# Optimization experiments

Measured on AMD Instinct MI355X. Metric: run time of the kernel, lower is better.

Reference implementation:

```python
import jax, jax.numpy as jnp
import numpy as np
from jax.scipy.special import logsumexp

TAU = 0.05
N_ITERS = 10
LR = 0.5
BETA1 = 0.9
BETA2 = 0.999
EPS_ADAM = 1e-8
BATCH, N, M = 16, 1024, 1024


def setup_inputs() -> dict:
    key = jax.random.key(0)
    k1, k2, k3 = jax.random.split(key, 3)
    log_alpha = jax.random.normal(k1, (BATCH, N, M), dtype=jnp.float32)
    # valid log-marginals (rows of log_alpha's transport plan must sum to exp(log_a))
    log_a = jax.nn.log_softmax(jax.random.normal(k2, (BATCH, N), dtype=jnp.float32), axis=-1)
    log_b = jax.nn.log_softmax(jax.random.normal(k3, (BATCH, M), dtype=jnp.float32), axis=-1)
    return {"log_alpha": log_alpha, "log_a": log_a, "log_b": log_b}


def _sinkhorn_adam(log_alpha, log_a, log_b):
    kernel = log_alpha / TAU  # [B, N, M]
    b, n, m = log_alpha.shape
    u = jnp.zeros((b, n), dtype=log_alpha.dtype)
    v = jnp.zeros((b, m), dtype=log_alpha.dtype)
    m_u = jnp.zeros_like(u)
    v_u = jnp.zeros_like(u)
    m_v = jnp.zeros_like(v)
    v_v = jnp.zeros_like(v)

    def step(carry, iter_idx):
        u, v, m_u, v_u, m_v, v_v = carry
        t = (iter_idx + 1).astype(log_alpha.dtype)
        bc1 = 1.0 - jnp.power(jnp.asarray(BETA1, log_alpha.dtype), t)
        bc2 = 1.0 - jnp.power(jnp.asarray(BETA2, log_alpha.dtype), t)

        # u update (Adam on the fixed-point residual)
        u_target = log_a - logsumexp(kernel + v[:, None, :], axis=-1)
        g_u = u_target - u
        m_u = BETA1 * m_u + (1.0 - BETA1) * g_u
        v_u = BETA2 * v_u + (1.0 - BETA2) * (g_u * g_u)
        u_next = u + LR * (m_u / bc1) / (jnp.sqrt(v_u / bc2) + EPS_ADAM)

        # v update using the fresh u
        v_target = log_b - logsumexp(kernel + u_next[:, :, None], axis=-2)
        g_v = v_target - v
        m_v = BETA1 * m_v + (1.0 - BETA1) * g_v
        v_v = BETA2 * v_v + (1.0 - BETA2) * (g_v * g_v)
        v_next = v + LR * (m_v / bc1) / (jnp.sqrt(v_v / bc2) + EPS_ADAM)

        return (u_next, v_next, m_u, v_u, m_v, v_v), None

    (u, v, m_u, v_u, m_v, v_v), _ = jax.lax.scan(
        step, (u, v, m_u, v_u, m_v, v_v), jnp.arange(N_ITERS))
    # transport plan
    return jnp.exp(kernel + u[:, :, None] + v[:, None, :])


def reference(log_alpha, log_a, log_b):
    return _sinkhorn_adam(log_alpha, log_a, log_b)
```

## Files before the change

kernel.cpp:

```cpp
#include <hip/hip_runtime.h>
#include <cmath>

#define BB 16
#define NN 1024
#define MM 1024
#define RPB 8
#define NSLAB (NN / RPB)

static constexpr float INV_TAU = 20.0f;
static constexpr float LR   = 0.5f;
static constexpr float B1f  = 0.9f;
static constexpr float B2f  = 0.999f;
static constexpr float EPSA = 1e-8f;
static constexpr float EXP_CAP = 88.0f;

#define OFF_U   0
#define OFF_V   16384
#define OFF_MU  32768
#define OFF_VU  49152
#define OFF_MV  65536
#define OFF_VV  81920
#define OFF_PART 98304

__global__ void init_state(float* __restrict__ ws) {
    int i = blockIdx.x * 256 + threadIdx.x;
    ws[i] = 0.0f;
}

__global__ __launch_bounds__(256, 4) void iter_fused(
    const float* __restrict__ la, const float* __restrict__ log_a,
    float* __restrict__ ws, float2* __restrict__ part,
    float bc1, float bc2)
{
    const int slab = blockIdx.x;
    const int b    = blockIdx.y;
    const int row0 = slab * RPB;
    const int tid  = threadIdx.x;
    const int wave = tid >> 6;
    const int lane = tid & 63;
    __shared__ float redm[4 * RPB];
    __shared__ float reds[4 * RPB];
    __shared__ float fin[RPB];
    __shared__ float su[RPB];

    const float* Kb = la + ((size_t)b * NN + row0) * MM + 4 * tid;
    float kr[RPB][4];
#pragma unroll
    for (int r = 0; r < RPB; ++r) {
        const float4 k4 = *(const float4*)(Kb + (size_t)r * MM);
        kr[r][0] = k4.x * INV_TAU; kr[r][1] = k4.y * INV_TAU;
        kr[r][2] = k4.z * INV_TAU; kr[r][3] = k4.w * INV_TAU;
    }
    const float4 v4 = *(const float4*)(ws + OFF_V + b * MM + 4 * tid);
    const float vj[4] = {v4.x, v4.y, v4.z, v4.w};

    float pm[RPB];
#pragma unroll
    for (int r = 0; r < RPB; ++r)
        pm[r] = fmaxf(fmaxf(kr[r][0] + vj[0], kr[r][1] + vj[1]),
                      fmaxf(kr[r][2] + vj[2], kr[r][3] + vj[3]));
#pragma unroll
    for (int off = 32; off; off >>= 1)
#pragma unroll
        for (int r = 0; r < RPB; ++r)
            pm[r] = fmaxf(pm[r], __shfl_xor(pm[r], off, 64));
    if (lane == 0)
#pragma unroll
        for (int r = 0; r < RPB; ++r) redm[wave * RPB + r] = pm[r];
    __syncthreads();
    if (tid < RPB)
        fin[tid] = fmaxf(fmaxf(redm[tid], redm[RPB + tid]),
                         fmaxf(redm[2 * RPB + tid], redm[3 * RPB + tid]));
    __syncthreads();
    float Mr[RPB];
#pragma unroll
    for (int r = 0; r < RPB; ++r) Mr[r] = fin[r];

    float ps[RPB];
#pragma unroll
    for (int r = 0; r < RPB; ++r)
        ps[r] = __expf(kr[r][0] + vj[0] - Mr[r]) + __expf(kr[r][1] + vj[1] - Mr[r])
              + __expf(kr[r][2] + vj[2] - Mr[r]) + __expf(kr[r][3] + vj[3] - Mr[r]);
#pragma unroll
    for (int off = 32; off; off >>= 1)
#pragma unroll
        for (int r = 0; r < RPB; ++r)
            ps[r] += __shfl_xor(ps[r], off, 64);
    if (lane == 0)
#pragma unroll
        for (int r = 0; r < RPB; ++r) reds[wave * RPB + r] = ps[r];
    __syncthreads();
    if (tid < RPB) {
        const int r  = tid;
        const int gi = b * NN + row0 + r;
        const float S   = reds[r] + reds[RPB + r] + reds[2 * RPB + r] + reds[3 * RPB + r];
        const float lse = Mr[r] + __logf(S);
        const float uo  = ws[OFF_U + gi];
        const float gu  = (log_a[gi] - lse) - uo;
        const float m_  = B1f * ws[OFF_MU + gi] + (1.f - B1f) * gu;
        const float v_  = B2f * ws[OFF_VU + gi] + (1.f - B2f) * gu * gu;
        ws[OFF_MU + gi] = m_;
        ws[OFF_VU + gi] = v_;
        const float un  = uo + LR * (m_ / bc1) / (sqrtf(v_ / bc2) + EPSA);
        ws[OFF_U + gi]  = un;
        su[r] = un;
    }
    __syncthreads();
    float uu[RPB];
#pragma unroll
    for (int r = 0; r < RPB; ++r) uu[r] = su[r];

    float2 out4[4];
#pragma unroll
    for (int j = 0; j < 4; ++j) {
        float m = kr[0][j] + uu[0];
#pragma unroll
        for (int r = 1; r < RPB; ++r) m = fmaxf(m, kr[r][j] + uu[r]);
        float s = 0.f;
#pragma unroll
        for (int r = 0; r < RPB; ++r) s += __expf(kr[r][j] + uu[r] - m);
        out4[j] = make_float2(m, s);
    }
    float2* p = part + ((size_t)b * NSLAB + slab) * MM + 4 * tid;
    p[0] = out4[0]; p[1] = out4[1]; p[2] = out4[2]; p[3] = out4[3];
}

__global__ __launch_bounds__(256, 8) void combine(
    const float* __restrict__ log_b, float* __restrict__ ws,
    const float2* __restrict__ part, float bc1, float bc2)
{
    const int b   = blockIdx.x >> 4;
    const int mg  = blockIdx.x & 15;
    const int tid = threadIdx.x;
    const int c   = tid & 63;
    const int q   = tid >> 6;
    const int m   = mg * 64 + c;
    __shared__ float2 red[4][64];

    const float2* p = part + ((size_t)b * NSLAB + q * 32) * MM + m;
    float M = -3.0e38f, S = 0.f;
#pragma unroll 8
    for (int s = 0; s < 32; ++s) {
        const float2 pr = p[(size_t)s * MM];
        const float mn = fmaxf(M, pr.x);
        S = S * __expf(M - mn) + pr.y * __expf(pr.x - mn);
        M = mn;
    }
    red[q][c] = make_float2(M, S);
    __syncthreads();
    if (q == 0) {
        const float2 a = red[0][c], bb = red[1][c], cc = red[2][c], d = red[3][c];
        const float Mt = fmaxf(fmaxf(a.x, bb.x), fmaxf(cc.x, d.x));
        const float St = a.y * __expf(a.x - Mt) + bb.y * __expf(bb.x - Mt)
                       + cc.y * __expf(cc.x - Mt) + d.y * __expf(d.x - Mt);
        const int i = b * MM + m;
        const float lse = Mt + __logf(St);
        const float vo  = ws[OFF_V + i];
        const float gv  = (log_b[i] - lse) - vo;
        const float m_  = B1f * ws[OFF_MV + i] + (1.f - B1f) * gv;
        const float v_  = B2f * ws[OFF_VV + i] + (1.f - B2f) * gv * gv;
        ws[OFF_MV + i] = m_;
        ws[OFF_VV + i] = v_;
        ws[OFF_V + i]  = vo + LR * (m_ / bc1) / (sqrtf(v_ / bc2) + EPSA);
    }
}

__global__ void finalize(const float* __restrict__ la, const float* __restrict__ ws,
                         float* __restrict__ out)
{
    const size_t i4 = (size_t)blockIdx.x * 256 + threadIdx.x;
    const size_t e  = i4 * 4;
    const int row = (int)(e >> 10);
    const int b   = row >> 10;
    const int m   = (int)(e & 1023);
    const float uu = ws[OFF_U + row];
    const float4 k4 = ((const float4*)la)[i4];
    const float4 v4 = *(const float4*)(ws + OFF_V + b * MM + m);
    float4 o;
    o.x = __expf(fminf(k4.x * INV_TAU + uu + v4.x, EXP_CAP));
    o.y = __expf(fminf(k4.y * INV_TAU + uu + v4.y, EXP_CAP));
    o.z = __expf(fminf(k4.z * INV_TAU + uu + v4.z, EXP_CAP));
    o.w = __expf(fminf(k4.w * INV_TAU + uu + v4.w, EXP_CAP));
    ((float4*)out)[i4] = o;
}

extern "C" void kernel_launch(void* const* d_in, const int* in_sizes, int n_in,
                              void* d_out, int out_size, void* d_ws, size_t ws_size,
                              hipStream_t stream) {
    const float* la    = (const float*)d_in[0];
    const float* log_a = (const float*)d_in[1];
    const float* log_b = (const float*)d_in[2];
    float*  out  = (float*)d_out;
    float*  ws   = (float*)d_ws;
    float2* part = (float2*)(ws + OFF_PART);

    init_state<<<384, 256, 0, stream>>>(ws);
    for (int t = 1; t <= 10; ++t) {
        const float bc1 = 1.0f - powf(B1f, (float)t);
        const float bc2 = 1.0f - powf(B2f, (float)t);
        iter_fused<<<dim3(NSLAB, BB), 256, 0, stream>>>(la, log_a, ws, part, bc1, bc2);
        combine<<<BB * MM / 256, 256, 0, stream>>>(log_b, ws, part, bc1, bc2);
    }
    finalize<<<16384, 256, 0, stream>>>(la, ws, out);
}
```

Measured before the change: 340.1 us.

## Fuse column combine into next iteration with redundant per-slab v merge

```diff
diff --git a/kernel.cpp b/kernel.cpp
--- a/kernel.cpp
+++ b/kernel.cpp
@@ -4,8 +4,9 @@
 #define BB 16
 #define NN 1024
 #define MM 1024
-#define RPB 8
-#define NSLAB (NN / RPB)
+#define RPB 32
+#define NSLAB 32
+#define GR 8
 
 static constexpr float INV_TAU = 20.0f;
 static constexpr float LR   = 0.5f;
@@ -14,174 +15,211 @@
 static constexpr float EPSA = 1e-8f;
 static constexpr float EXP_CAP = 88.0f;
 
-#define OFF_U   0
-#define OFF_V   16384
-#define OFF_MU  32768
-#define OFF_VU  49152
-#define OFF_MV  65536
-#define OFF_VV  81920
-#define OFF_PART 98304
+#define OFF_U    0
+#define OFF_MU   16384
+#define OFF_VU   32768
+#define OFF_VST  49152
+#define OFF_PS0  (OFF_VST + BB*NSLAB*3*MM)
+#define OFF_PS1  (OFF_PS0 + BB*NSLAB*MM)
+#define OFF_PM0  (OFF_PS1 + BB*NSLAB*MM)
+#define OFF_PM1  (OFF_PM0 + BB*NSLAB)
 
 __global__ void init_state(float* __restrict__ ws) {
     int i = blockIdx.x * 256 + threadIdx.x;
     ws[i] = 0.0f;
 }
 
-__global__ __launch_bounds__(256, 4) void iter_fused(
+__device__ __forceinline__ void merge_v(
+    const float* __restrict__ pS, const float* __restrict__ pM,
+    const float* __restrict__ log_b, float* __restrict__ vstp,
+    float* vsh, float* fsh, float* mgsh,
+    int b, int tid, int lane, float bcv1, float bcv2)
+{
+    if ((tid >> 6) == 0) {
+        const float m = pM[b * NSLAB + (lane & 31)];
+        float M = m;
+#pragma unroll
+        for (int off = 16; off; off >>= 1)
+            M = fmaxf(M, __shfl_xor(M, off, 64));
+        if (lane < 32) fsh[lane] = __expf(m - M);
+        if (lane == 0) *mgsh = M;
+    }
+    __syncthreads();
+    const float* ps = pS + (size_t)b * NSLAB * MM + tid;
+    float acc = 0.f;
+#pragma unroll
+    for (int s = 0; s < NSLAB; ++s)
+        acc = __builtin_fmaf(ps[(size_t)s * MM], fsh[s], acc);
+    const float lse = *mgsh + __logf(acc);
+    const float vo = vstp[0], mo = vstp[MM], wo = vstp[2 * MM];
+    const float gv = (log_b[b * MM + tid] - lse) - vo;
+    const float mn = B1f * mo + (1.f - B1f) * gv;
+    const float wn = B2f * wo + (1.f - B2f) * gv * gv;
+    const float vn = vo + LR * (mn / bcv1) / (sqrtf(wn / bcv2) + EPSA);
+    vstp[0] = vn; vstp[MM] = mn; vstp[2 * MM] = wn;
+    vsh[tid] = vn;
+}
+
+__global__ __launch_bounds__(1024, 4) void iter_kernel(
     const float* __restrict__ la, const float* __restrict__ log_a,
-    float* __restrict__ ws, float2* __restrict__ part,
-    float bc1, float bc2)
+    const float* __restrict__ log_b, float* __restrict__ ws,
+    const float* __restrict__ pSr, const float* __restrict__ pMr,
+    float* __restrict__ pSw, float* __restrict__ pMw,
+    int t, float bcu1, float bcu2, float bcv1, float bcv2)
 {
     const int slab = blockIdx.x;
     const int b    = blockIdx.y;
-    const int row0 = slab * RPB;
     const int tid  = threadIdx.x;
-    const int wave = tid >> 6;
+    const int g    = tid >> 8;
+    const int gt   = tid & 255;
     const int lane = tid & 63;
-    __shared__ float redm[4 * RPB];
-    __shared__ float reds[4 * RPB];
-    __shared__ float fin[RPB];
-    __shared__ float su[RPB];
-
-    const float* Kb = la + ((size_t)b * NN + row0) * MM + 4 * tid;
-    float kr[RPB][4];
-#pragma unroll
-    for (int r = 0; r < RPB; ++r) {
+    const int gwave = (tid >> 6) & 3;
+
+    __shared__ float vsh[MM];
+    __shared__ float fsh[NSLAB];
+    __shared__ float redm[4][4][GR];
+    __shared__ float reds[4][4][GR];
+    __shared__ float rowm[4][GR];
+    __shared__ float suh[4][GR];
+    __shared__ float mgsh;
+    __shared__ float Sp[4][MM];
+
+    float* vstp = ws + OFF_VST + (size_t)(b * NSLAB + slab) * 3 * MM + tid;
+    if (t > 1)
+        merge_v(pSr, pMr, log_b, vstp, vsh, fsh, &mgsh, b, tid, lane, bcv1, bcv2);
+    else
+        vsh[tid] = 0.f;
+    __syncthreads();
+
+    const int row0 = slab * RPB + g * GR;
+    const float* Kb = la + ((size_t)(b * NN + row0)) * MM + 4 * gt;
+    float kr[GR][4];
+#pragma unroll
+    for (int r = 0; r < GR; ++r) {
         const float4 k4 = *(const float4*)(Kb + (size_t)r * MM);
         kr[r][0] = k4.x * INV_TAU; kr[r][1] = k4.y * INV_TAU;
         kr[r][2] = k4.z * INV_TAU; kr[r][3] = k4.w * INV_TAU;
     }
-    const float4 v4 = *(const float4*)(ws + OFF_V + b * MM + 4 * tid);
+    const float4 v4 = *(const float4*)(vsh + 4 * gt);
     const float vj[4] = {v4.x, v4.y, v4.z, v4.w};
 
-    float pm[RPB];
-#pragma unroll
-    for (int r = 0; r < RPB; ++r)
+    float pm[GR];
+#pragma unroll
+    for (int r = 0; r < GR; ++r)
         pm[r] = fmaxf(fmaxf(kr[r][0] + vj[0], kr[r][1] + vj[1]),
                       fmaxf(kr[r][2] + vj[2], kr[r][3] + vj[3]));
 #pragma unroll
     for (int off = 32; off; off >>= 1)
 #pragma unroll
-        for (int r = 0; r < RPB; ++r)
+        for (int r = 0; r < GR; ++r)
             pm[r] = fmaxf(pm[r], __shfl_xor(pm[r], off, 64));
     if (lane == 0)
 #pragma unroll
-        for (int r = 0; r < RPB; ++r) redm[wave * RPB + r] = pm[r];
-    __syncthreads();
-    if (tid < RPB)
-        fin[tid] = fmaxf(fmaxf(redm[tid], redm[RPB + tid]),
-                         fmaxf(redm[2 * RPB + tid], redm[3 * RPB + tid]));
-    __syncthreads();
-    float Mr[RPB];
-#pragma unroll
-    for (int r = 0; r < RPB; ++r) Mr[r] = fin[r];
-
-    float ps[RPB];
-#pragma unroll
-    for (int r = 0; r < RPB; ++r)
+        for (int r = 0; r < GR; ++r) redm[g][gwave][r] = pm[r];
+    __syncthreads();
+    if (gt < GR)
+        rowm[g][gt] = fmaxf(fmaxf(redm[g][0][gt], redm[g][1][gt]),
+                            fmaxf(redm[g][2][gt], redm[g][3][gt]));
+    __syncthreads();
+    float Mr[GR];
+#pragma unroll
+    for (int r = 0; r < GR; ++r) Mr[r] = rowm[g][r];
+
+    float ps[GR];
+#pragma unroll
+    for (int r = 0; r < GR; ++r)
         ps[r] = __expf(kr[r][0] + vj[0] - Mr[r]) + __expf(kr[r][1] + vj[1] - Mr[r])
               + __expf(kr[r][2] + vj[2] - Mr[r]) + __expf(kr[r][3] + vj[3] - Mr[r]);
 #pragma unroll
     for (int off = 32; off; off >>= 1)
 #pragma unroll
-        for (int r = 0; r < RPB; ++r)
+        for (int r = 0; r < GR; ++r)
             ps[r] += __shfl_xor(ps[r], off, 64);
     if (lane == 0)
 #pragma unroll
-        for (int r = 0; r < RPB; ++r) reds[wave * RPB + r] = ps[r];
-    __syncthreads();
-    if (tid < RPB) {
-        const int r  = tid;
+        for (int r = 0; r < GR; ++r) reds[g][gwave][r] = ps[r];
+    __syncthreads();
+    if (gt < GR) {
+        const int r  = gt;
         const int gi = b * NN + row0 + r;
-        const float S   = reds[r] + reds[RPB + r] + reds[2 * RPB + r] + reds[3 * RPB + r];
-        const float lse = Mr[r] + __logf(S);
+        const float S   = reds[g][0][r] + reds[g][1][r] + reds[g][2][r] + reds[g][3][r];
+        const float lse = rowm[g][r] + __logf(S);
         const float uo  = ws[OFF_U + gi];
         const float gu  = (log_a[gi] - lse) - uo;
         const float m_  = B1f * ws[OFF_MU + gi] + (1.f - B1f) * gu;
-        const float v_  = B2f * ws[OFF_VU + gi] + (1.f - B2f) * gu * gu;
+        const float w_  = B2f * ws[OFF_VU + gi] + (1.f - B2f) * gu * gu;
         ws[OFF_MU + gi] = m_;
-        ws[OFF_VU + gi] = v_;
-        const float un  = uo + LR * (m_ / bc1) / (sqrtf(v_ / bc2) + EPSA);
+        ws[OFF_VU + gi] = w_;
+        const float un  = uo + LR * (m_ / bcu1) / (sqrtf(w_ / bcu2) + EPSA);
         ws[OFF_U + gi]  = un;
-        su[r] = un;
-    }
-    __syncthreads();
-    float uu[RPB];
-#pragma unroll
-    for (int r = 0; r < RPB; ++r) uu[r] = su[r];
-
-    float2 out4[4];
+        suh[g][r] = un;
+    }
+    __syncthreads();
+
+    if ((tid >> 6) == 0) {
+        const int idx = lane & 31;
+        float m = rowm[idx >> 3][idx & 7] + suh[idx >> 3][idx & 7];
+#pragma unroll
+        for (int off = 16; off; off >>= 1)
+            m = fmaxf(m, __shfl_xor(m, off, 64));
+        if (lane == 0) mgsh = m;
+    }
+    __syncthreads();
+    const float msl = mgsh;
+
+    float uu[GR];
+#pragma unroll
+    for (int r = 0; r < GR; ++r) uu[r] = suh[g][r];
+    float s4[4];
 #pragma unroll
     for (int j = 0; j < 4; ++j) {
-        float m = kr[0][j] + uu[0];
-#pragma unroll
-        for (int r = 1; r < RPB; ++r) m = fmaxf(m, kr[r][j] + uu[r]);
         float s = 0.f;
 #pragma unroll
-        for (int r = 0; r < RPB; ++r) s += __expf(kr[r][j] + uu[r] - m);
-        out4[j] = make_float2(m, s);
-    }
-    float2* p = part + ((size_t)b * NSLAB + slab) * MM + 4 * tid;
-    p[0] = out4[0]; p[1] = out4[1]; p[2] = out4[2]; p[3] = out4[3];
-}
-
-__global__ __launch_bounds__(256, 8) void combine(
-    const float* __restrict__ log_b, float* __restrict__ ws,
-    const float2* __restrict__ part, float bc1, float bc2)
+        for (int r = 0; r < GR; ++r) s += __expf(kr[r][j] + uu[r] - msl);
+        s4[j] = s;
+    }
+    *(float4*)(Sp[g] + 4 * gt) = make_float4(s4[0], s4[1], s4[2], s4[3]);
+    __syncthreads();
+    pSw[(size_t)(b * NSLAB + slab) * MM + tid]
+        = Sp[0][tid] + Sp[1][tid] + Sp[2][tid] + Sp[3][tid];
+    if (tid == 0) pMw[b * NSLAB + slab] = msl;
+}
+
+__global__ __launch_bounds__(1024, 4) void fin_kernel(
+    const float* __restrict__ la, const float* __restrict__ log_b,
+    float* __restrict__ ws,
+    const float* __restrict__ pSr, const float* __restrict__ pMr,
+    float* __restrict__ out, float bcv1, float bcv2)
 {
-    const int b   = blockIdx.x >> 4;
-    const int mg  = blockIdx.x & 15;
-    const int tid = threadIdx.x;
-    const int c   = tid & 63;
-    const int q   = tid >> 6;
-    const int m   = mg * 64 + c;
-    __shared__ float2 red[4][64];
-
-    const float2* p = part + ((size_t)b * NSLAB + q * 32) * MM + m;
-    float M = -3.0e38f, S = 0.f;
-#pragma unroll 8
-    for (int s = 0; s < 32; ++s) {
-        const float2 pr = p[(size_t)s * MM];
-        const float mn = fmaxf(M, pr.x);
-        S = S * __expf(M - mn) + pr.y * __expf(pr.x - mn);
-        M = mn;
-    }
-    red[q][c] = make_float2(M, S);
-    __syncthreads();
-    if (q == 0) {
-        const float2 a = red[0][c], bb = red[1][c], cc = red[2][c], d = red[3][c];
-        const float Mt = fmaxf(fmaxf(a.x, bb.x), fmaxf(cc.x, d.x));
-        const float St = a.y * __expf(a.x - Mt) + bb.y * __expf(bb.x - Mt)
-                       + cc.y * __expf(cc.x - Mt) + d.y * __expf(d.x - Mt);
-        const int i = b * MM + m;
-        const float lse = Mt + __logf(St);
-        const float vo  = ws[OFF_V + i];
-        const float gv  = (log_b[i] - lse) - vo;
-        const float m_  = B1f * ws[OFF_MV + i] + (1.f - B1f) * gv;
-        const float v_  = B2f * ws[OFF_VV + i] + (1.f - B2f) * gv * gv;
-        ws[OFF_MV + i] = m_;
-        ws[OFF_VV + i] = v_;
-        ws[OFF_V + i]  = vo + LR * (m_ / bc1) / (sqrtf(v_ / bc2) + EPSA);
-    }
-}
-
-__global__ void finalize(const float* __restrict__ la, const float* __restrict__ ws,
-                         float* __restrict__ out)
-{
-    const size_t i4 = (size_t)blockIdx.x * 256 + threadIdx.x;
-    const size_t e  = i4 * 4;
-    const int row = (int)(e >> 10);
-    const int b   = row >> 10;
-    const int m   = (int)(e & 1023);
-    const float uu = ws[OFF_U + row];
-    const float4 k4 = ((const float4*)la)[i4];
-    const float4 v4 = *(const float4*)(ws + OFF_V + b * MM + m);
-    float4 o;
-    o.x = __expf(fminf(k4.x * INV_TAU + uu + v4.x, EXP_CAP));
-    o.y = __expf(fminf(k4.y * INV_TAU + uu + v4.y, EXP_CAP));
-    o.z = __expf(fminf(k4.z * INV_TAU + uu + v4.z, EXP_CAP));
-    o.w = __expf(fminf(k4.w * INV_TAU + uu + v4.w, EXP_CAP));
-    ((float4*)out)[i4] = o;
+    const int slab = blockIdx.x;
+    const int b    = blockIdx.y;
+    const int tid  = threadIdx.x;
+    const int g    = tid >> 8;
+    const int gt   = tid & 255;
+    const int lane = tid & 63;
+    __shared__ float vsh[MM];
+    __shared__ float fsh[NSLAB];
+    __shared__ float mgsh;
+
+    float* vstp = ws + OFF_VST + (size_t)(b * NSLAB + slab) * 3 * MM + tid;
+    merge_v(pSr, pMr, log_b, vstp, vsh, fsh, &mgsh, b, tid, lane, bcv1, bcv2);
+    __syncthreads();
+
+    const int row0 = slab * RPB + g * GR;
+    const float4 v4 = *(const float4*)(vsh + 4 * gt);
+    const float* Kb = la + ((size_t)(b * NN + row0)) * MM + 4 * gt;
+    float* Ob = out + ((size_t)(b * NN + row0)) * MM + 4 * gt;
+#pragma unroll
+    for (int r = 0; r < GR; ++r) {
+        const float u = ws[OFF_U + b * NN + row0 + r];
+        const float4 k4 = *(const float4*)(Kb + (size_t)r * MM);
+        float4 o;
+        o.x = __expf(fminf(k4.x * INV_TAU + u + v4.x, EXP_CAP));
+        o.y = __expf(fminf(k4.y * INV_TAU + u + v4.y, EXP_CAP));
+        o.z = __expf(fminf(k4.z * INV_TAU + u + v4.z, EXP_CAP));
+        o.w = __expf(fminf(k4.w * INV_TAU + u + v4.w, EXP_CAP));
+        *(float4*)(Ob + (size_t)r * MM) = o;
+    }
 }
 
 extern "C" void kernel_launch(void* const* d_in, const int* in_sizes, int n_in,
@@ -190,16 +228,23 @@
     const float* la    = (const float*)d_in[0];
     const float* log_a = (const float*)d_in[1];
     const float* log_b = (const float*)d_in[2];
-    float*  out  = (float*)d_out;
-    float*  ws   = (float*)d_ws;
-    float2* part = (float2*)(ws + OFF_PART);
-
-    init_state<<<384, 256, 0, stream>>>(ws);
+    float* out = (float*)d_out;
+    float* ws  = (float*)d_ws;
+    float* PS[2] = {ws + OFF_PS0, ws + OFF_PS1};
+    float* PM[2] = {ws + OFF_PM0, ws + OFF_PM1};
+
+    init_state<<<6336, 256, 0, stream>>>(ws);
     for (int t = 1; t <= 10; ++t) {
-        const float bc1 = 1.0f - powf(B1f, (float)t);
-        const float bc2 = 1.0f - powf(B2f, (float)t);
-        iter_fused<<<dim3(NSLAB, BB), 256, 0, stream>>>(la, log_a, ws, part, bc1, bc2);
-        combine<<<BB * MM / 256, 256, 0, stream>>>(log_b, ws, part, bc1, bc2);
-    }
-    finalize<<<16384, 256, 0, stream>>>(la, ws, out);
-}
+        const float bcu1 = 1.f - powf(B1f, (float)t);
+        const float bcu2 = 1.f - powf(B2f, (float)t);
+        const float bcv1 = (t > 1) ? 1.f - powf(B1f, (float)(t - 1)) : 1.f;
+        const float bcv2 = (t > 1) ? 1.f - powf(B2f, (float)(t - 1)) : 1.f;
+        iter_kernel<<<dim3(NSLAB, BB), 1024, 0, stream>>>(
+            la, log_a, log_b, ws,
+            PS[(t - 1) & 1], PM[(t - 1) & 1], PS[t & 1], PM[t & 1],
+            t, bcu1, bcu2, bcv1, bcv2);
+    }
+    fin_kernel<<<dim3(NSLAB, BB), 1024, 0, stream>>>(
+        la, log_b, ws, PS[0], PM[0], out,
+        1.f - powf(B1f, 10.0f), 1.f - powf(B2f, 10.0f));
+}
```

Result: slower. 409.8 us (+20.5%).
